# Optimization experiments

Hardware: AMD Instinct MI355X
Metric: run time of the kernel (lower is better)

## Reference

```python
import jax, jax.numpy as jnp
import numpy as np

B, F, D = 4096, 39, 16          # batch, num_field, embedding_size
V = 1000000                     # num_feat (vocab)
H1, H2 = 128, 128               # cin_layer_sizes
INPUT_DIM = F * D               # 624
FC_DIM = H1 // 2 + H2           # 192 (split_half)
DEEP = [400, 400]
BN_EPS = 1e-5


def setup_inputs() -> dict:
    key = jax.random.key(0)
    ks = jax.random.split(key, 16)
    xav = lambda k, shp: jax.random.normal(k, shp, jnp.float32) * np.sqrt(2.0 / (shp[0] + shp[-1]))
    return {
        "feat_index": jax.random.randint(ks[0], (B, F), 0, V),
        "feat_value": jax.random.uniform(ks[1], (B, F), jnp.float32),
        "emb_table": xav(ks[2], (V, D)),
        "linear_w": xav(ks[3], (INPUT_DIM, 1)),
        "linear_b": jnp.zeros((1,), jnp.float32),
        "conv_w1": xav(ks[4], (H1, F, F)),          # (out, h_prev, m) == conv1d 1x1 weight reshaped
        "conv_b1": jnp.zeros((H1,), jnp.float32),
        "conv_w2": xav(ks[5], (H2, H1 // 2, F)),
        "conv_b2": jnp.zeros((H2,), jnp.float32),
        "deep_w1": xav(ks[6], (INPUT_DIM, DEEP[0])),
        "deep_b1": jnp.zeros((DEEP[0],), jnp.float32),
        "bn_g1": jnp.ones((DEEP[0],), jnp.float32),
        "bn_b1": jnp.zeros((DEEP[0],), jnp.float32),
        "deep_w2": xav(ks[7], (DEEP[0], DEEP[1])),
        "deep_b2": jnp.zeros((DEEP[1],), jnp.float32),
        "bn_g2": jnp.ones((DEEP[1],), jnp.float32),
        "bn_b2": jnpp if False else jnp.zeros((DEEP[1],), jnp.float32),
        "out_w": xav(ks[8], (1 + FC_DIM + DEEP[1], 1)),
        "out_b": jnp.zeros((1,), jnp.float32),
    }


def _bn(x, g, b):
    # torch BatchNorm1d in training mode: biased batch variance
    m = x.mean(axis=0)
    v = x.var(axis=0)
    return g * (x - m) * jax.lax.rsqrt(v + BN_EPS) + b


def reference(feat_index, feat_value, emb_table, linear_w, linear_b,
              conv_w1, conv_b1, conv_w2, conv_b2,
              deep_w1, deep_b1, bn_g1, bn_b1,
              deep_w2, deep_b2, bn_g2, bn_b2,
              out_w, out_b):
    e = emb_table[feat_index]                      # [B, F, D]
    flat = e.reshape(e.shape[0], -1)               # [B, F*D]
    linear_part = flat @ linear_w + linear_b       # [B, 1]

    # CIN: fused outer-product + 1x1 conv (x_k[b,o,d] = sum_{h,m} W[o,h,m] x_prev[b,h,d] x0[b,m,d])
    x0 = e
    h1 = jax.nn.relu(jnp.einsum('bhd,bmd,ohm->bod', x0, x0, conv_w1) + conv_b1[None, :, None])
    nxt, hi1 = jnp.split(h1, 2, axis=1)            # split_half
    h2 = jax.nn.relu(jnp.einsum('bhd,bmd,ohm->bod', nxt, x0, conv_w2) + conv_b2[None, :, None])
    res = jnp.concatenate([hi1, h2], axis=1).sum(axis=2)   # [B, FC_DIM]

    # Deep tower (dropout off / deterministic)
    y = jax.nn.relu(_bn(flat @ deep_w1 + deep_b1, bn_g1, bn_b1))
    y = jax.nn.relu(_bn(y @ deep_w2 + deep_b2, bn_g2, bn_b2))

    cat = jnp.concatenate([linear_part, res, y], axis=1)   # [B, 593]
    return cat @ out_w + out_b
```

## Files before the change

kernel.cpp:

```cpp
#include <hip/hip_runtime.h>

#define BATCH   4096
#define NF      39
#define ED      16
#define IN_DIM  624
#define DW      400
#define BN_EPS  1e-5f
#define NK16    156
#define AK1     640
#define NKS1    20
#define NKS2    13
#define WCOL    416

typedef __attribute__((ext_vector_type(8))) short short8;
typedef __attribute__((ext_vector_type(16))) float f32x16;
typedef __attribute__((ext_vector_type(4))) float f32x4;
typedef __attribute__((ext_vector_type(2))) float f32x2;
typedef unsigned short u16;

__device__ inline unsigned pack_hi2(float a, float b) {
  return __builtin_amdgcn_perm(__float_as_uint(b), __float_as_uint(a), 0x07060302u);
}
__device__ inline unsigned bf16_rne(float f) {
  unsigned u = __float_as_uint(f);
  u += 0x7fff + ((u >> 16) & 1);
  return u >> 16;
}
__device__ inline float bf2f(u16 v) { return __uint_as_float((unsigned)v << 16); }

#define CIN_E (NK16 * 128 * 16)
#define D1_E  (NKS1 * WCOL * 32)
#define D2_E  (NKS2 * WCOL * 32)
#define PREP_E (CIN_E + D1_E + D2_E + 1600)
#define PREP_B ((PREP_E + 255) / 256)
#define GATH_B (BATCH / 4)

__global__ __launch_bounds__(256) void k_gp(const int* __restrict__ idx,
    const float* __restrict__ emb, const float* __restrict__ lw,
    const float* __restrict__ lb, const float* __restrict__ w1,
    const float* __restrict__ w2, const float* __restrict__ dw1,
    const float* __restrict__ dw2, u16* __restrict__ flatb,
    float* __restrict__ lp, u16* __restrict__ wp1, u16* __restrict__ wp2,
    u16* __restrict__ wpd1, u16* __restrict__ wpd2, float* __restrict__ gstat) {
  int t = threadIdx.x;
  if (blockIdx.x < GATH_B) {
    int lane = t & 63;
    int b = blockIdx.x * 4 + (t >> 6);
    int sj = (lane < NF) ? idx[b * NF + lane] : 0;
    float acc = 0.f;
#pragma unroll
    for (int i = 0; i < 10; i++) {
      int e = lane + i * 64;
      if (e < IN_DIM) {
        int f = e >> 4;
        int row = __shfl(sj, f);
        float v = emb[(size_t)row * ED + (e & 15)];
        flatb[(size_t)b * AK1 + e] = (u16)bf16_rne(v);
        acc = fmaf(v, lw[e], acc);
      } else {
        flatb[(size_t)b * AK1 + e] = 0;
      }
    }
#pragma unroll
    for (int k = 1; k < 64; k <<= 1) acc += __shfl_xor(acc, k);
    if (lane == 0) lp[b] = acc + lb[0];
  } else {
    int e = (blockIdx.x - GATH_B) * 256 + t;
    if (e < CIN_E) {
      int k16 = e >> 11, r = e & 2047, col = r >> 4, kk = r & 15;
      int k = k16 * 16 + kk, h = k & 63, m = k >> 6;
      float v1 = (h < NF) ? w1[(size_t)col * (NF * NF) + h * NF + m] : 0.f;
      float v2 = w2[(size_t)col * (64 * NF) + h * NF + m];
      wp1[e] = (u16)bf16_rne(v1);
      wp2[e] = (u16)bf16_rne(v2);
    } else if (e < CIN_E + D1_E) {
      int e2 = e - CIN_E;
      int ksg = e2 / (WCOL * 32), r = e2 - ksg * (WCOL * 32);
      int col = r >> 5, kk = r & 31;
      int k = ksg * 32 + kk;
      wpd1[e2] = (k < IN_DIM && col < DW) ? (u16)bf16_rne(dw1[(size_t)k * DW + col]) : 0;
    } else if (e < CIN_E + D1_E + D2_E) {
      int e2 = e - CIN_E - D1_E;
      int ksg = e2 / (WCOL * 32), r = e2 - ksg * (WCOL * 32);
      int col = r >> 5, kk = r & 31;
      int k = ksg * 32 + kk;
      wpd2[e2] = (k < DW && col < DW) ? (u16)bf16_rne(dw2[(size_t)k * DW + col]) : 0;
    } else if (e < PREP_E) {
      gstat[e - CIN_E - D1_E - D2_E] = 0.f;
    }
  }
}

template <bool LAY2>
__global__ __launch_bounds__(256, 2) void k_cin32(
    const u16* __restrict__ flatb, const u16* __restrict__ nxtg,
    const u16* __restrict__ wp, const float* __restrict__ bias,
    u16* __restrict__ nxt_out, float* __restrict__ res) {
  int t = threadIdx.x;
  int w = t >> 6, lane = t & 63;
  int col = lane & 31, khalf = lane >> 5;
  int si = (lane >> 4) & 1, d = lane & 15;
  int b0 = blockIdx.x * 8 + w * 2;
  int b = b0 + si;
  const u16* fb = flatb + (size_t)b * AK1;

  f32x2 sp[4][4];
  if (LAY2) {
#pragma unroll
    for (int s = 0; s < 4; s++) {
      uint4 v = *(const uint4*)(nxtg + (((size_t)b * 16 + d) * 64 + s * 16 + khalf * 8));
      unsigned uu[4] = {v.x, v.y, v.z, v.w};
#pragma unroll
      for (int w4 = 0; w4 < 4; w4++)
        sp[s][w4] = (f32x2){__uint_as_float(uu[w4] << 16),
                            __uint_as_float(uu[w4] & 0xffff0000u)};
    }
  } else {
#pragma unroll
    for (int s = 0; s < 4; s++)
#pragma unroll
      for (int w4 = 0; w4 < 4; w4++) {
        int h0 = s * 16 + khalf * 8 + 2 * w4;
        int h1 = h0 + 1;
        float f0 = (h0 < NF) ? bf2f(fb[h0 * 16 + d]) : 0.f;
        float f1 = (h1 < NF) ? bf2f(fb[h1 * 16 + d]) : 0.f;
        sp[s][w4] = (f32x2){f0, f1};
      }
  }

  f32x16 acc[4];
#pragma unroll
  for (int nt = 0; nt < 4; nt++)
#pragma unroll
    for (int r = 0; r < 16; r++) acc[nt][r] = 0.f;

  const u16* wbase = wp + (size_t)col * 16 + khalf * 8;
  short8 bfr[3][4];
#pragma unroll
  for (int nt = 0; nt < 4; nt++) {
    bfr[0][nt] = *(const short8*)(wbase + nt * 512);
    bfr[1][nt] = *(const short8*)(wbase + 2048 + nt * 512);
  }

  float xv = bf2f(fb[d]);
  float xvn;

  for (int mg = 0; mg < 13; mg++) {
#pragma unroll
    for (int j = 0; j < 12; j++) {
      int k16 = mg * 12 + j;
      if (j == 0 || j == 4 || j == 8) {
        int mn = mg * 3 + (j >> 2) + 1;
        xvn = bf2f(fb[mn * 16 + d]);
      }
      if (j < 10 || mg < 12) {
        const u16* wb = wbase + (size_t)(k16 + 2) * 2048;
#pragma unroll
        for (int nt = 0; nt < 4; nt++)
          bfr[(j + 2) % 3][nt] = *(const short8*)(wb + nt * 512);
      }
      int s = j & 3;
      union { unsigned u[4]; short8 v; } a;
      f32x2 xv2 = (f32x2){xv, xv};
#pragma unroll
      for (int w4 = 0; w4 < 4; w4++) {
        f32x2 p = sp[s][w4] * xv2;
        a.u[w4] = pack_hi2(p[0], p[1]);
      }
#pragma unroll
      for (int nt = 0; nt < 4; nt++)
        acc[nt] = __builtin_amdgcn_mfma_f32_32x32x16_bf16(
            a.v, bfr[j % 3][nt], acc[nt], 0, 0, 0);
      if (s == 3) xv = xvn;
    }
  }

#pragma unroll
  for (int nt = 0; nt < 4; nt++) {
    int o = nt * 32 + col;
    float bi = bias[o];
    if (!LAY2 && nt < 2) {
#pragma unroll
      for (int r = 0; r < 16; r++) {
        int si2 = r >> 3;
        int dd = (r & 3) + 8 * ((r >> 2) & 1) + 4 * khalf;
        float v = fmaxf(acc[nt][r] + bi, 0.f);
        nxt_out[((size_t)(b0 + si2) * 16 + dd) * 64 + o] = (u16)bf16_rne(v);
      }
    } else {
      float p0 = 0.f, p1 = 0.f;
#pragma unroll
      for (int r = 0; r < 8; r++)  p0 += fmaxf(acc[nt][r] + bi, 0.f);
#pragma unroll
      for (int r = 8; r < 16; r++) p1 += fmaxf(acc[nt][r] + bi, 0.f);
      p0 += __shfl_xor(p0, 32);
      p1 += __shfl_xor(p1, 32);
      if (khalf == 0) {
        int ri = LAY2 ? (64 + o) : (o - 64);
        res[(size_t)b0 * 192 + ri] = p0;
        res[(size_t)(b0 + 1) * 192 + ri] = p1;
      }
    }
  }
}

template <bool BN_A, int NKS, int KREAL, int AK>
__global__ __launch_bounds__(256) void k_gemm_mfma(
    const u16* __restrict__ Abf, const float* __restrict__ Af32,
    const u16* __restrict__ wp, const float* __restrict__ bias,
    const float* __restrict__ gsIn, const float* __restrict__ gs2In,
    const float* __restrict__ bng, const float* __restrict__ bnb,
    float* __restrict__ C, float* __restrict__ gs, float* __restrict__ gs2) {
  __shared__ float lsS[NKS * 32], lsH[NKS * 32];
  __shared__ float lred[64];
  int t = threadIdx.x;
  if (BN_A) {
    for (int c = t; c < NKS * 32; c += 256) {
      float sc = 0.f, sh = 0.f;
      if (c < DW) {
        float m = gsIn[c] * (1.f / BATCH);
        float var = gs2In[c] * (1.f / BATCH) - m * m;
        sc = bng[c] * rsqrtf(var + BN_EPS);
        sh = bnb[c] - m * sc;
      }
      lsS[c] = sc; lsH[c] = sh;
    }
  }
  if (t < 64) lred[t] = 0.f;
  __syncthreads();

  int w = t >> 6, lane = t & 63;
  int nl = lane & 15, q = lane >> 4;
  int row = blockIdx.x * 64 + w * 16 + nl;
  int c0 = blockIdx.y * 32;
  f32x4 acc[2];
  acc[0] = (f32x4){0.f, 0.f, 0.f, 0.f};
  acc[1] = (f32x4){0.f, 0.f, 0.f, 0.f};

  short8 araw[2]; f32x4 fraw0[2], fraw1[2]; short8 braw[2][2];
  auto loadA_raw = [&](int ksg, int buf) {
    int kb = ksg * 32 + q * 8;
    if (!BN_A) {
      araw[buf] = *(const short8*)(Abf + (size_t)row * AK + kb);
    } else {
      if (kb + 8 <= KREAL) {
        fraw0[buf] = *(const f32x4*)(Af32 + (size_t)row * KREAL + kb);
        fraw1[buf] = *(const f32x4*)(Af32 + (size_t)row * KREAL + kb + 4);
      } else {
        fraw0[buf] = (f32x4){0.f,0.f,0.f,0.f};
        fraw1[buf] = (f32x4){0.f,0.f,0.f,0.f};
      }
    }
    const u16* wb = wp + (size_t)ksg * (WCOL * 32) + (size_t)(c0 + nl) * 32 + q * 8;
    braw[buf][0] = *(const short8*)wb;
    braw[buf][1] = *(const short8*)(wb + 16 * 32);
  };
  auto cookA = [&](int ksg, int buf) -> short8 {
    if (!BN_A) return araw[buf];
    int kb = ksg * 32 + q * 8;
    f32x4 s0 = *(const f32x4*)&lsS[kb], h0 = *(const f32x4*)&lsH[kb];
    f32x4 s1 = *(const f32x4*)&lsS[kb + 4], h1 = *(const f32x4*)&lsH[kb + 4];
    union { unsigned u[4]; short8 s; } a;
    float v0 = fmaxf(fmaf(fraw0[buf][0], s0[0], h0[0]), 0.f);
    float v1 = fmaxf(fmaf(fraw0[buf][1], s0[1], h0[1]), 0.f);
    float v2 = fmaxf(fmaf(fraw0[buf][2], s0[2], h0[2]), 0.f);
    float v3 = fmaxf(fmaf(fraw0[buf][3], s0[3], h0[3]), 0.f);
    float v4 = fmaxf(fmaf(fraw1[buf][0], s1[0], h1[0]), 0.f);
    float v5 = fmaxf(fmaf(fraw1[buf][1], s1[1], h1[1]), 0.f);
    float v6 = fmaxf(fmaf(fraw1[buf][2], s1[2], h1[2]), 0.f);
    float v7 = fmaxf(fmaf(fraw1[buf][3], s1[3], h1[3]), 0.f);
    a.u[0] = bf16_rne(v0) | (bf16_rne(v1) << 16);
    a.u[1] = bf16_rne(v2) | (bf16_rne(v3) << 16);
    a.u[2] = bf16_rne(v4) | (bf16_rne(v5) << 16);
    a.u[3] = bf16_rne(v6) | (bf16_rne(v7) << 16);
    return a.s;
  };

  loadA_raw(0, 0);
#pragma unroll 4
  for (int ksg = 0; ksg < NKS; ksg++) {
    int cur = ksg & 1;
    if (ksg + 1 < NKS) loadA_raw(ksg + 1, cur ^ 1);
    short8 afr = cookA(ksg, cur);
    acc[0] = __builtin_amdgcn_mfma_f32_16x16x32_bf16(afr, braw[cur][0], acc[0], 0, 0, 0);
    acc[1] = __builtin_amdgcn_mfma_f32_16x16x32_bf16(afr, braw[cur][1], acc[1], 0, 0, 0);
  }

  int rbase = blockIdx.x * 64 + w * 16 + q * 4;
#pragma unroll
  for (int nt = 0; nt < 2; nt++) {
    int col = c0 + nt * 16 + nl;
    if (col < DW) {
      float bi = bias[col];
      float s = 0.f, s2 = 0.f;
#pragma unroll
      for (int r = 0; r < 4; r++) {
        float v = acc[nt][r] + bi;
        C[(size_t)(rbase + r) * DW + col] = v;
        s += v; s2 = fmaf(v, v, s2);
      }
      s += __shfl_xor(s, 16); s2 += __shfl_xor(s2, 16);
      s += __shfl_xor(s, 32); s2 += __shfl_xor(s2, 32);
      if (q == 0) {
        atomicAdd(&lred[nt * 16 + nl], s);
        atomicAdd(&lred[32 + nt * 16 + nl], s2);
      }
    }
  }
  __syncthreads();
  if (t < 32) {
    int col = c0 + t;
    if (col < DW) atomicAdd(&gs[col], lred[t]);
  } else if (t < 64) {
    int col = c0 + t - 32;
    if (col < DW) atomicAdd(&gs2[col], lred[t]);
  }
}

__global__ __launch_bounds__(256) void k_final(const float* __restrict__ lp,
    const float* __restrict__ res, const float* __restrict__ y2,
    const float* __restrict__ gB, const float* __restrict__ gB2,
    const float* __restrict__ g2, const float* __restrict__ bb2,
    const float* __restrict__ ow, const float* __restrict__ ob,
    float* __restrict__ out) {
  __shared__ float lsS[DW], lsH[DW];
  int t = threadIdx.x;
  for (int c = t; c < DW; c += 256) {
    float m = gB[c] * (1.f / BATCH);
    float var = gB2[c] * (1.f / BATCH) - m * m;
    float sc = g2[c] * rsqrtf(var + BN_EPS);
    lsS[c] = sc;
    lsH[c] = bb2[c] - m * sc;
  }
  __syncthreads();
  int lane = t & 63, w = t >> 6;
  int b = blockIdx.x * 4 + w;
  float acc = 0.f;
  for (int j = lane; j < 593; j += 64) {
    float v;
    if (j == 0)       v = lp[b];
    else if (j < 193) v = res[(size_t)b * 192 + (j - 1)];
    else {
      int c = j - 193;
      v = fmaxf(fmaf(y2[(size_t)b * DW + c], lsS[c], lsH[c]), 0.f);
    }
    acc = fmaf(v, ow[j], acc);
  }
#pragma unroll
  for (int k = 1; k < 64; k <<= 1) acc += __shfl_xor(acc, k);
  if (lane == 0) out[b] = acc + ob[0];
}

extern "C" void kernel_launch(void* const* d_in, const int* in_sizes, int n_in,
                              void* d_out, int out_size, void* d_ws, size_t ws_size,
                              hipStream_t stream) {
  const int*   feat_index = (const int*)d_in[0];
  const float* emb = (const float*)d_in[2];
  const float* lw  = (const float*)d_in[3];
  const float* lb  = (const float*)d_in[4];
  const float* w1  = (const float*)d_in[5];
  const float* b1  = (const float*)d_in[6];
  const float* w2  = (const float*)d_in[7];
  const float* b2  = (const float*)d_in[8];
  const float* dw1 = (const float*)d_in[9];
  const float* db1 = (const float*)d_in[10];
  const float* g1  = (const float*)d_in[11];
  const float* bb1 = (const float*)d_in[12];
  const float* dw2 = (const float*)d_in[13];
  const float* db2 = (const float*)d_in[14];
  const float* g2  = (const float*)d_in[15];
  const float* bb2 = (const float*)d_in[16];
  const float* ow  = (const float*)d_in[17];
  const float* ob  = (const float*)d_in[18];

  float* ws   = (float*)d_ws;
  u16*  flatb = (u16*)ws;
  float* y1   = ws + 1310720;
  float* res  = ws + 2949120;
  float* lp   = ws + 3735552;
  float* gA   = ws + 3741248;
  float* gA2  = gA + 400;
  float* gB   = gA2 + 400;
  float* gB2  = gB + 400;
  u16*  nxtg  = (u16*)(ws + 3742848);
  float* y2   = ws + 3742848;
  u16*  wp1   = (u16*)(ws + 5840000);
  u16*  wp2   = (u16*)(ws + 5999744);
  u16*  wpd1  = (u16*)(ws + 6159488);
  u16*  wpd2  = (u16*)(ws + 6292608);
  float* out  = (float*)d_out;

  k_gp<<<GATH_B + PREP_B, 256, 0, stream>>>(feat_index, emb, lw, lb, w1, w2,
      dw1, dw2, flatb, lp, wp1, wp2, wpd1, wpd2, gA);
  k_cin32<false><<<512, 256, 0, stream>>>(flatb, nullptr, wp1, b1, nxtg, res);
  k_cin32<true><<<512, 256, 0, stream>>>(flatb, nxtg, wp2, b2, nullptr, res);
  k_gemm_mfma<false, NKS1, IN_DIM, AK1><<<dim3(BATCH / 64, 13), 256, 0, stream>>>(
      flatb, nullptr, wpd1, db1, nullptr, nullptr, nullptr, nullptr, y1, gA, gA2);
  k_gemm_mfma<true, NKS2, DW, 0><<<dim3(BATCH / 64, 13), 256, 0, stream>>>(
      nullptr, y1, wpd2, db2, gA, gA2, g1, bb1, y2, gB, gB2);
  k_final<<<BATCH / 4, 256, 0, stream>>>(lp, res, y2, gB, gB2, g2, bb2, ow, ob, out);
}
```

Before: 271.7 us.

## Fuse both CIN layers into one kernel with shared-memory intermediate

Merges the two CIN layer kernels into one. Layer-1 activations pass through a swizzled LDS buffer instead of a global round trip. Layer 1 now uses a compact weight packing that skips the padded h rows (117 K-steps instead of 156). The work split changes so each wave handles 4 samples and 64 output channels. It also adds s_setprio around the MFMA blocks and deepens the layer-2 weight prefetch, at the cost of more registers and a block-wide barrier.

New measurement: 246.9 us (median of 2 runs). -9.1%, faster.

```diff
diff --git a/kernel.cpp b/kernel.cpp
--- a/kernel.cpp
+++ b/kernel.cpp
@@ -6,11 +6,12 @@
 #define IN_DIM  624
 #define DW      400
 #define BN_EPS  1e-5f
-#define NK16    156
 #define AK1     640
 #define NKS1    20
 #define NKS2    13
 #define WCOL    416
+#define NK1     117
+#define NK2     156
 
 typedef __attribute__((ext_vector_type(8))) short short8;
 typedef __attribute__((ext_vector_type(16))) float f32x16;
@@ -28,10 +29,11 @@
 }
 __device__ inline float bf2f(u16 v) { return __uint_as_float((unsigned)v << 16); }
 
-#define CIN_E (NK16 * 128 * 16)
+#define CIN1_E (NK1 * 2048)
+#define CIN2_E (NK2 * 2048)
 #define D1_E  (NKS1 * WCOL * 32)
 #define D2_E  (NKS2 * WCOL * 32)
-#define PREP_E (CIN_E + D1_E + D2_E + 1600)
+#define PREP_E (CIN1_E + CIN2_E + D1_E + D2_E + 1600)
 #define PREP_B ((PREP_E + 255) / 256)
 #define GATH_B (BATCH / 4)
 
@@ -66,142 +68,245 @@
     if (lane == 0) lp[b] = acc + lb[0];
   } else {
     int e = (blockIdx.x - GATH_B) * 256 + t;
-    if (e < CIN_E) {
+    if (e < CIN1_E) {
       int k16 = e >> 11, r = e & 2047, col = r >> 4, kk = r & 15;
+      int mg = k16 / 3, sg = k16 - mg * 3;
+      int h = sg * 16 + kk;
+      wp1[e] = (h < NF) ? (u16)bf16_rne(w1[(size_t)col * (NF * NF) + h * NF + mg])
+                        : (u16)0;
+    } else if (e < CIN1_E + CIN2_E) {
+      int e2 = e - CIN1_E;
+      int k16 = e2 >> 11, r = e2 & 2047, col = r >> 4, kk = r & 15;
       int k = k16 * 16 + kk, h = k & 63, m = k >> 6;
-      float v1 = (h < NF) ? w1[(size_t)col * (NF * NF) + h * NF + m] : 0.f;
-      float v2 = w2[(size_t)col * (64 * NF) + h * NF + m];
-      wp1[e] = (u16)bf16_rne(v1);
-      wp2[e] = (u16)bf16_rne(v2);
-    } else if (e < CIN_E + D1_E) {
-      int e2 = e - CIN_E;
+      wp2[e2] = (u16)bf16_rne(w2[(size_t)col * (64 * NF) + h * NF + m]);
+    } else if (e < CIN1_E + CIN2_E + D1_E) {
+      int e2 = e - CIN1_E - CIN2_E;
       int ksg = e2 / (WCOL * 32), r = e2 - ksg * (WCOL * 32);
       int col = r >> 5, kk = r & 31;
       int k = ksg * 32 + kk;
       wpd1[e2] = (k < IN_DIM && col < DW) ? (u16)bf16_rne(dw1[(size_t)k * DW + col]) : 0;
-    } else if (e < CIN_E + D1_E + D2_E) {
-      int e2 = e - CIN_E - D1_E;
+    } else if (e < CIN1_E + CIN2_E + D1_E + D2_E) {
+      int e2 = e - CIN1_E - CIN2_E - D1_E;
       int ksg = e2 / (WCOL * 32), r = e2 - ksg * (WCOL * 32);
       int col = r >> 5, kk = r & 31;
       int k = ksg * 32 + kk;
       wpd2[e2] = (k < DW && col < DW) ? (u16)bf16_rne(dw2[(size_t)k * DW + col]) : 0;
     } else if (e < PREP_E) {
-      gstat[e - CIN_E - D1_E - D2_E] = 0.f;
-    }
-  }
-}
-
-template <bool LAY2>
-__global__ __launch_bounds__(256, 2) void k_cin32(
-    const u16* __restrict__ flatb, const u16* __restrict__ nxtg,
-    const u16* __restrict__ wp, const float* __restrict__ bias,
-    u16* __restrict__ nxt_out, float* __restrict__ res) {
+      gstat[e - CIN1_E - CIN2_E - D1_E - D2_E] = 0.f;
+    }
+  }
+}
+
+__global__ __launch_bounds__(256, 2) void k_cin_f(
+    const u16* __restrict__ flatb, const u16* __restrict__ wp1,
+    const u16* __restrict__ wp2, const float* __restrict__ bias1,
+    const float* __restrict__ bias2, float* __restrict__ res) {
+  __shared__ __align__(16) u16 s1b[8 * 16 * 64];
   int t = threadIdx.x;
   int w = t >> 6, lane = t & 63;
+  int sgrp = w & 1, oh = w >> 1;
   int col = lane & 31, khalf = lane >> 5;
   int si = (lane >> 4) & 1, d = lane & 15;
-  int b0 = blockIdx.x * 8 + w * 2;
-  int b = b0 + si;
-  const u16* fb = flatb + (size_t)b * AK1;
-
-  f32x2 sp[4][4];
-  if (LAY2) {
-#pragma unroll
-    for (int s = 0; s < 4; s++) {
-      uint4 v = *(const uint4*)(nxtg + (((size_t)b * 16 + d) * 64 + s * 16 + khalf * 8));
-      unsigned uu[4] = {v.x, v.y, v.z, v.w};
-#pragma unroll
-      for (int w4 = 0; w4 < 4; w4++)
-        sp[s][w4] = (f32x2){__uint_as_float(uu[w4] << 16),
-                            __uint_as_float(uu[w4] & 0xffff0000u)};
-    }
-  } else {
-#pragma unroll
-    for (int s = 0; s < 4; s++)
+  int b0 = blockIdx.x * 8 + sgrp * 4;
+  const u16* fb = flatb + (size_t)(b0 + si) * AK1;
+
+  f32x2 sp1[2][3][4];
+#pragma unroll
+  for (int p = 0; p < 2; p++)
+#pragma unroll
+    for (int s = 0; s < 3; s++)
 #pragma unroll
       for (int w4 = 0; w4 < 4; w4++) {
         int h0 = s * 16 + khalf * 8 + 2 * w4;
         int h1 = h0 + 1;
-        float f0 = (h0 < NF) ? bf2f(fb[h0 * 16 + d]) : 0.f;
-        float f1 = (h1 < NF) ? bf2f(fb[h1 * 16 + d]) : 0.f;
-        sp[s][w4] = (f32x2){f0, f1};
-      }
-  }
-
-  f32x16 acc[4];
-#pragma unroll
-  for (int nt = 0; nt < 4; nt++)
-#pragma unroll
-    for (int r = 0; r < 16; r++) acc[nt][r] = 0.f;
-
-  const u16* wbase = wp + (size_t)col * 16 + khalf * 8;
-  short8 bfr[3][4];
-#pragma unroll
-  for (int nt = 0; nt < 4; nt++) {
-    bfr[0][nt] = *(const short8*)(wbase + nt * 512);
-    bfr[1][nt] = *(const short8*)(wbase + 2048 + nt * 512);
-  }
-
-  float xv = bf2f(fb[d]);
-  float xvn;
-
+        float f0 = (h0 < NF) ? bf2f(fb[p * 1280 + h0 * 16 + d]) : 0.f;
+        float f1 = (h1 < NF) ? bf2f(fb[p * 1280 + h1 * 16 + d]) : 0.f;
+        sp1[p][s][w4] = (f32x2){f0, f1};
+      }
+
+  const u16* wb1 = wp1 + (size_t)(oh * 64 + col) * 16 + khalf * 8;
+  short8 bfr[3][2];
+#pragma unroll
+  for (int k16 = 0; k16 < 2; k16++)
+#pragma unroll
+    for (int nt = 0; nt < 2; nt++)
+      bfr[k16][nt] = *(const short8*)(wb1 + (size_t)k16 * 2048 + nt * 512);
+
+  f32x16 acc[2][2];
+#pragma unroll
+  for (int p = 0; p < 2; p++)
+#pragma unroll
+    for (int nt = 0; nt < 2; nt++)
+#pragma unroll
+      for (int r = 0; r < 16; r++) acc[p][nt][r] = 0.f;
+
+  float xv[2] = {bf2f(fb[d]), bf2f(fb[1280 + d])};
+  float xvn[2];
+
+#pragma unroll 1
+  for (int mg = 0; mg < 13; mg++) {
+#pragma unroll
+    for (int j = 0; j < 9; j++) {
+      int k16 = mg * 9 + j;
+      int s = j % 3;
+      if (s == 0) {
+        int mn = mg * 3 + j / 3 + 1;
+        xvn[0] = bf2f(fb[mn * 16 + d]);
+        xvn[1] = bf2f(fb[1280 + mn * 16 + d]);
+      }
+      {
+        const u16* wbp = wb1 + (size_t)(k16 + 2) * 2048;
+#pragma unroll
+        for (int nt = 0; nt < 2; nt++)
+          bfr[(s + 2) % 3][nt] = *(const short8*)(wbp + nt * 512);
+      }
+      __builtin_amdgcn_s_setprio(1);
+#pragma unroll
+      for (int p = 0; p < 2; p++) {
+        union { unsigned u[4]; short8 v; } a;
+        f32x2 xv2 = (f32x2){xv[p], xv[p]};
+#pragma unroll
+        for (int w4 = 0; w4 < 4; w4++) {
+          f32x2 pr = sp1[p][s][w4] * xv2;
+          a.u[w4] = pack_hi2(pr[0], pr[1]);
+        }
+#pragma unroll
+        for (int nt = 0; nt < 2; nt++)
+          acc[p][nt] = __builtin_amdgcn_mfma_f32_32x32x16_bf16(
+              a.v, bfr[s][nt], acc[p][nt], 0, 0, 0);
+      }
+      __builtin_amdgcn_s_setprio(0);
+      if (s == 2) { xv[0] = xvn[0]; xv[1] = xvn[1]; }
+    }
+  }
+
+  if (oh == 0) {
+#pragma unroll
+    for (int p = 0; p < 2; p++)
+#pragma unroll
+      for (int nt = 0; nt < 2; nt++) {
+        int o = nt * 32 + col;
+        float bi = bias1[o];
+#pragma unroll
+        for (int r = 0; r < 16; r++) {
+          int smp = sgrp * 4 + p * 2 + (r >> 3);
+          int dd = (r & 3) + 8 * ((r >> 2) & 1) + 4 * khalf;
+          float v = fmaxf(acc[p][nt][r] + bi, 0.f);
+          int ix = (((smp * 16 + dd) * 64) + o) ^ ((dd & 7) << 3);
+          s1b[ix] = (u16)bf16_rne(v);
+        }
+      }
+  } else {
+#pragma unroll
+    for (int p = 0; p < 2; p++)
+#pragma unroll
+      for (int nt = 0; nt < 2; nt++) {
+        int o = 64 + nt * 32 + col;
+        float bi = bias1[o];
+        float p0 = 0.f, p1 = 0.f;
+#pragma unroll
+        for (int r = 0; r < 8; r++)  p0 += fmaxf(acc[p][nt][r] + bi, 0.f);
+#pragma unroll
+        for (int r = 8; r < 16; r++) p1 += fmaxf(acc[p][nt][r] + bi, 0.f);
+        p0 += __shfl_xor(p0, 32);
+        p1 += __shfl_xor(p1, 32);
+        if (khalf == 0) {
+          res[(size_t)(b0 + p * 2) * 192 + (o - 64)] = p0;
+          res[(size_t)(b0 + p * 2 + 1) * 192 + (o - 64)] = p1;
+        }
+      }
+  }
+
+  const u16* wb2 = wp2 + (size_t)(oh * 64 + col) * 16 + khalf * 8;
+  short8 bq[4][2];
+#pragma unroll
+  for (int k16 = 0; k16 < 3; k16++)
+#pragma unroll
+    for (int nt = 0; nt < 2; nt++)
+      bq[k16][nt] = *(const short8*)(wb2 + (size_t)k16 * 2048 + nt * 512);
+
+  __syncthreads();
+
+  f32x2 sp2[2][4][4];
+#pragma unroll
+  for (int p = 0; p < 2; p++) {
+    int smp = sgrp * 4 + p * 2 + si;
+#pragma unroll
+    for (int s = 0; s < 4; s++) {
+      int ix = ((smp * 16 + d) * 64 + s * 16 + khalf * 8) ^ ((d & 7) << 3);
+      union { short8 v; u16 e[8]; } vv;
+      vv.v = *(const short8*)(s1b + ix);
+#pragma unroll
+      for (int w4 = 0; w4 < 4; w4++)
+        sp2[p][s][w4] = (f32x2){bf2f(vv.e[2 * w4]), bf2f(vv.e[2 * w4 + 1])};
+    }
+  }
+
+#pragma unroll
+  for (int p = 0; p < 2; p++)
+#pragma unroll
+    for (int nt = 0; nt < 2; nt++)
+#pragma unroll
+      for (int r = 0; r < 16; r++) acc[p][nt][r] = 0.f;
+
+  xv[0] = bf2f(fb[d]);
+  xv[1] = bf2f(fb[1280 + d]);
+
+#pragma unroll 1
   for (int mg = 0; mg < 13; mg++) {
 #pragma unroll
     for (int j = 0; j < 12; j++) {
       int k16 = mg * 12 + j;
-      if (j == 0 || j == 4 || j == 8) {
+      int s = j & 3;
+      if (s == 0) {
         int mn = mg * 3 + (j >> 2) + 1;
-        xvn = bf2f(fb[mn * 16 + d]);
-      }
-      if (j < 10 || mg < 12) {
-        const u16* wb = wbase + (size_t)(k16 + 2) * 2048;
-#pragma unroll
-        for (int nt = 0; nt < 4; nt++)
-          bfr[(j + 2) % 3][nt] = *(const short8*)(wb + nt * 512);
-      }
-      int s = j & 3;
-      union { unsigned u[4]; short8 v; } a;
-      f32x2 xv2 = (f32x2){xv, xv};
-#pragma unroll
-      for (int w4 = 0; w4 < 4; w4++) {
-        f32x2 p = sp[s][w4] * xv2;
-        a.u[w4] = pack_hi2(p[0], p[1]);
-      }
-#pragma unroll
-      for (int nt = 0; nt < 4; nt++)
-        acc[nt] = __builtin_amdgcn_mfma_f32_32x32x16_bf16(
-            a.v, bfr[j % 3][nt], acc[nt], 0, 0, 0);
-      if (s == 3) xv = xvn;
-    }
-  }
-
-#pragma unroll
-  for (int nt = 0; nt < 4; nt++) {
-    int o = nt * 32 + col;
-    float bi = bias[o];
-    if (!LAY2 && nt < 2) {
-#pragma unroll
-      for (int r = 0; r < 16; r++) {
-        int si2 = r >> 3;
-        int dd = (r & 3) + 8 * ((r >> 2) & 1) + 4 * khalf;
-        float v = fmaxf(acc[nt][r] + bi, 0.f);
-        nxt_out[((size_t)(b0 + si2) * 16 + dd) * 64 + o] = (u16)bf16_rne(v);
-      }
-    } else {
+        xvn[0] = bf2f(fb[mn * 16 + d]);
+        xvn[1] = bf2f(fb[1280 + mn * 16 + d]);
+      }
+      {
+        const u16* wbp = wb2 + (size_t)(k16 + 3) * 2048;
+#pragma unroll
+        for (int nt = 0; nt < 2; nt++)
+          bq[(j + 3) & 3][nt] = *(const short8*)(wbp + nt * 512);
+      }
+      __builtin_amdgcn_s_setprio(1);
+#pragma unroll
+      for (int p = 0; p < 2; p++) {
+        union { unsigned u[4]; short8 v; } a;
+        f32x2 xv2 = (f32x2){xv[p], xv[p]};
+#pragma unroll
+        for (int w4 = 0; w4 < 4; w4++) {
+          f32x2 pr = sp2[p][s][w4] * xv2;
+          a.u[w4] = pack_hi2(pr[0], pr[1]);
+        }
+#pragma unroll
+        for (int nt = 0; nt < 2; nt++)
+          acc[p][nt] = __builtin_amdgcn_mfma_f32_32x32x16_bf16(
+              a.v, bq[s][nt], acc[p][nt], 0, 0, 0);
+      }
+      __builtin_amdgcn_s_setprio(0);
+      if (s == 3) { xv[0] = xvn[0]; xv[1] = xvn[1]; }
+    }
+  }
+
+#pragma unroll
+  for (int p = 0; p < 2; p++)
+#pragma unroll
+    for (int nt = 0; nt < 2; nt++) {
+      int o = oh * 64 + nt * 32 + col;
+      float bi = bias2[o];
       float p0 = 0.f, p1 = 0.f;
 #pragma unroll
-      for (int r = 0; r < 8; r++)  p0 += fmaxf(acc[nt][r] + bi, 0.f);
-#pragma unroll
-      for (int r = 8; r < 16; r++) p1 += fmaxf(acc[nt][r] + bi, 0.f);
+      for (int r = 0; r < 8; r++)  p0 += fmaxf(acc[p][nt][r] + bi, 0.f);
+#pragma unroll
+      for (int r = 8; r < 16; r++) p1 += fmaxf(acc[p][nt][r] + bi, 0.f);
       p0 += __shfl_xor(p0, 32);
       p1 += __shfl_xor(p1, 32);
       if (khalf == 0) {
-        int ri = LAY2 ? (64 + o) : (o - 64);
-        res[(size_t)b0 * 192 + ri] = p0;
-        res[(size_t)(b0 + 1) * 192 + ri] = p1;
-      }
-    }
-  }
+        res[(size_t)(b0 + p * 2) * 192 + 64 + o] = p0;
+        res[(size_t)(b0 + p * 2 + 1) * 192 + 64 + o] = p1;
+      }
+    }
 }
 
 template <bool BN_A, int NKS, int KREAL, int AK>
@@ -382,18 +487,16 @@
   float* gA2  = gA + 400;
   float* gB   = gA2 + 400;
   float* gB2  = gB + 400;
-  u16*  nxtg  = (u16*)(ws + 3742848);
   float* y2   = ws + 3742848;
-  u16*  wp1   = (u16*)(ws + 5840000);
-  u16*  wp2   = (u16*)(ws + 5999744);
-  u16*  wpd1  = (u16*)(ws + 6159488);
-  u16*  wpd2  = (u16*)(ws + 6292608);
+  u16*  wp1   = (u16*)(ws + 5381248);
+  u16*  wp2   = (u16*)(ws + 5501056);
+  u16*  wpd1  = (u16*)(ws + 5660800);
+  u16*  wpd2  = (u16*)(ws + 5793920);
   float* out  = (float*)d_out;
 
   k_gp<<<GATH_B + PREP_B, 256, 0, stream>>>(feat_index, emb, lw, lb, w1, w2,
       dw1, dw2, flatb, lp, wp1, wp2, wpd1, wpd2, gA);
-  k_cin32<false><<<512, 256, 0, stream>>>(flatb, nullptr, wp1, b1, nxtg, res);
-  k_cin32<true><<<512, 256, 0, stream>>>(flatb, nxtg, wp2, b2, nullptr, res);
+  k_cin_f<<<512, 256, 0, stream>>>(flatb, wp1, wp2, b1, b2, res);
   k_gemm_mfma<false, NKS1, IN_DIM, AK1><<<dim3(BATCH / 64, 13), 256, 0, stream>>>(
       flatb, nullptr, wpd1, db1, nullptr, nullptr, nullptr, nullptr, y1, gA, gA2);
   k_gemm_mfma<true, NKS2, DW, 0><<<dim3(BATCH / 64, 13), 256, 0, stream>>>(
```
